# Kernel tuning notes

Hardware: AMD Instinct MI355X
Metric: run time of the kernel (lower is better)

The kernel has to match this reference:

```python
import jax, jax.numpy as jnp
import numpy as np

LN_EPS = 1e-12

def setup_inputs() -> dict:
    key = jax.random.key(0)
    k1, k2 = jax.random.split(key)
    B, S, H = 32, 2048, 1024
    input_tensor = jax.random.normal(k1, (B, S, H), dtype=jnp.float32)
    # learned params
    complex_weight = jax.random.normal(k2, (1, S // 2 + 1, H, 2), dtype=jnp.float32) * 0.02
    ln_gamma = jnp.ones((H,), dtype=jnp.float32)
    ln_beta = jnp.zeros((H,), dtype=jnp.float32)
    return {"input_tensor": input_tensor, "complex_weight": complex_weight,
            "ln_gamma": ln_gamma, "ln_beta": ln_beta}

def reference(input_tensor, complex_weight, ln_gamma, ln_beta):
    B, S, H = input_tensor.shape
    # FFT filter: rfft along seq, complex elementwise multiply, irfft
    x = jnp.fft.rfft(input_tensor, axis=1, norm='ortho')            # [B, S//2+1, H] complex64
    weight = complex_weight[..., 0] + 1j * complex_weight[..., 1]   # [1, S//2+1, H]
    x = x * weight
    seq_fft = jnp.fft.irfft(x, n=S, axis=1, norm='ortho')           # [B, S, H] real
    # dropout is identity in eval mode
    h = seq_fft + input_tensor
    # LayerNorm over last dim, eps=1e-12, biased variance (torch semantics)
    mean = jnp.mean(h, axis=-1, keepdims=True)
    var = jnp.mean(jnp.square(h - mean), axis=-1, keepdims=True)
    normed = (h - mean) * jax.lax.rsqrt(var + LN_EPS)
    return normed * ln_gamma + ln_beta
```

## Files before the change

kernel.cpp:

```cpp
#include <hip/hip_runtime.h>
#include <math.h>


#define PI_F 3.14159265358979323846f
#define SW(c) ((c) ^ (((c) >> 4) & 15))

__device__ __forceinline__ float2 cadd(float2 a, float2 b){ return make_float2(a.x+b.x, a.y+b.y); }
__device__ __forceinline__ float2 csub(float2 a, float2 b){ return make_float2(a.x-b.x, a.y-b.y); }
__device__ __forceinline__ float2 cmul(float2 a, float2 b){ return make_float2(a.x*b.x - a.y*b.y, a.x*b.y + a.y*b.x); }

template<int L>
__device__ __forceinline__ void fwd_stage(float2* A, int j){
  constexpr int half = L >> 1;
  const float ang0 = -PI_F / (float)L;
  #pragma unroll
  for (int r = 0; r < 4; ++r){
    int g    = j + (r << 7);
    int blk  = g / half;
    int joff = g - blk * half;
    int i0   = blk * (2 * L) + joff;
    float2 u0 = A[SW(i0)];
    float2 u1 = A[SW(i0 + half)];
    float2 u2 = A[SW(i0 + L)];
    float2 u3 = A[SW(i0 + L + half)];
    float sn, cs; __sincosf(ang0 * (float)joff, &sn, &cs);
    float2 w1 = make_float2(cs, sn);
    float2 t0  = cadd(u0, u2);
    float2 d02 = csub(u0, u2);
    float2 t1  = cadd(u1, u3);
    float2 d13 = csub(u1, u3);
    float2 t2  = cmul(d02, w1);
    float2 tm  = cmul(d13, w1);
    float2 t3  = make_float2(tm.y, -tm.x);
    float2 w2  = cmul(w1, w1);
    A[SW(i0)]            = cadd(t0, t1);
    A[SW(i0 + half)]     = cmul(csub(t0, t1), w2);
    A[SW(i0 + L)]        = cadd(t2, t3);
    A[SW(i0 + L + half)] = cmul(csub(t2, t3), w2);
  }
}

template<int l>
__device__ __forceinline__ void inv_stage(float2* A, int j){
  const float angB = PI_F / (float)(2 * l);
  #pragma unroll
  for (int r = 0; r < 4; ++r){
    int g    = j + (r << 7);
    int blk  = g / l;
    int joff = g - blk * l;
    int base = blk * (4 * l);
    int i0 = base + joff;
    float2 u0 = A[SW(i0)];
    float2 u1 = A[SW(i0 + l)];
    float2 u2 = A[SW(i0 + 2*l)];
    float2 u3 = A[SW(i0 + 3*l)];
    float sn, cs; __sincosf(angB * (float)joff, &sn, &cs);
    float2 wB = make_float2(cs, sn);
    float2 w  = cmul(wB, wB);
    float2 a1 = cmul(u1, w);
    float2 b0 = cadd(u0, a1), b1 = csub(u0, a1);
    float2 a3 = cmul(u3, w);
    float2 b2 = cadd(u2, a3), b3 = csub(u2, a3);
    float2 t2 = cmul(b2, wB);
    float2 c0 = cadd(b0, t2), c2 = csub(b0, t2);
    float2 iwB = make_float2(-wB.y, wB.x);
    float2 t3 = cmul(b3, iwB);
    float2 c1 = cadd(b1, t3), c3 = csub(b1, t3);
    A[SW(i0)]       = c0;
    A[SW(i0 + l)]   = c1;
    A[SW(i0 + 2*l)] = c2;
    A[SW(i0 + 3*l)] = c3;
  }
}

__device__ __forceinline__ float2 fetchW(const float2* __restrict__ wT,
                                         const float2* __restrict__ cw,
                                         int useT, int h, int k){
  if (useT) return wT[(size_t)h * 1025 + k];
  float2 w = cw[(size_t)k * 1024 + h];
  const float inv = 1.0f / 2048.0f;
  return make_float2((w.x + 1.0f) * inv, w.y * inv);
}

__global__ void prep_w_kernel(const float2* __restrict__ cw, float2* __restrict__ wT){
  __shared__ float2 tile[32][33];
  int k0 = blockIdx.x * 32, h0 = blockIdx.y * 32;
  int tx = threadIdx.x, ty = threadIdx.y;
  #pragma unroll
  for (int r = 0; r < 4; ++r){
    int k = k0 + ty + 8 * r;
    if (k < 1025) tile[ty + 8*r][tx] = cw[(size_t)k * 1024 + (h0 + tx)];
  }
  __syncthreads();
  const float inv = 1.0f / 2048.0f;
  #pragma unroll
  for (int r = 0; r < 4; ++r){
    int h = h0 + ty + 8 * r;
    int k = k0 + tx;
    if (k < 1025){
      float2 w = tile[tx][ty + 8*r];
      wT[(size_t)h * 1025 + k] = make_float2((w.x + 1.0f) * inv, w.y * inv);
    }
  }
}

__global__ __launch_bounds__(512) void fft_filter_kernel(
    const float2* __restrict__ x,
    const float2* __restrict__ cw,
    const float2* __restrict__ wT,
    int useT,
    float2* __restrict__ out){
  __shared__ float2 lds[4][2048];
  const int t  = threadIdx.x;
  const int bx = blockIdx.x;
  const int b  = bx >> 7;
  const int pg = bx & 127;
  const int f  = t >> 7;
  const int j  = t & 127;
  float2* A = lds[f];

  {
    const int p4 = t & 3, srow = t >> 2;
    const size_t base = ((size_t)b * 2048) * 512 + (size_t)(pg * 4 + p4);
    #pragma unroll
    for (int it = 0; it < 16; ++it){
      int s = srow + (it << 7);
      lds[p4][SW(s)] = x[base + (size_t)s * 512];
    }
  }
  __syncthreads();

  fwd_stage<1024>(A, j); __syncthreads();
  fwd_stage<256>(A, j);  __syncthreads();
  fwd_stage<64>(A, j);   __syncthreads();
  fwd_stage<16>(A, j);   __syncthreads();
  fwd_stage<4>(A, j);    __syncthreads();
  #pragma unroll
  for (int r = 0; r < 8; ++r){
    int m = j + (r << 7);
    int ia = SW(2*m), ib = SW(2*m + 1);
    float2 u = A[ia], v = A[ib];
    A[ia] = cadd(u, v);
    A[ib] = csub(u, v);
  }
  __syncthreads();

  {
    const int hA = (pg << 3) + (f << 1);
    if (j == 0){
      float2 z0 = A[0];
      float2 wa = fetchW(wT, cw, useT, hA, 0);
      float2 wb = fetchW(wT, cw, useT, hA + 1, 0);
      A[0] = make_float2(z0.x * wa.x, z0.y * wb.x);
      int p1 = SW(1);
      float2 zn = A[p1];
      wa = fetchW(wT, cw, useT, hA, 1024);
      wb = fetchW(wT, cw, useT, hA + 1, 1024);
      A[p1] = make_float2(zn.x * wa.x, zn.y * wb.x);
    }
    #pragma unroll
    for (int r = 0; r < 8; ++r){
      int k = 1 + j + (r << 7);
      if (k < 1024){
        int kr = 2048 - k;
        int p1 = SW((int)(__brev((unsigned)k) >> 21));
        int p2 = SW((int)(__brev((unsigned)kr) >> 21));
        float2 Z1 = A[p1], Z2 = A[p2];
        float2 Xa = make_float2(0.5f*(Z1.x + Z2.x), 0.5f*(Z1.y - Z2.y));
        float2 Xb = make_float2(0.5f*(Z1.y + Z2.y), 0.5f*(Z2.x - Z1.x));
        float2 wa = fetchW(wT, cw, useT, hA, k);
        float2 wb = fetchW(wT, cw, useT, hA + 1, k);
        float2 Ya = cmul(Xa, wa);
        float2 Yb = cmul(Xb, wb);
        A[p1] = make_float2(Ya.x - Yb.y, Ya.y + Yb.x);
        A[p2] = make_float2(Ya.x + Yb.y, Yb.x - Ya.y);
      }
    }
  }
  __syncthreads();

  #pragma unroll
  for (int r = 0; r < 8; ++r){
    int m = j + (r << 7);
    int ia = SW(2*m), ib = SW(2*m + 1);
    float2 u = A[ia], v = A[ib];
    A[ia] = cadd(u, v);
    A[ib] = csub(u, v);
  }
  __syncthreads();
  inv_stage<2>(A, j);   __syncthreads();
  inv_stage<8>(A, j);   __syncthreads();
  inv_stage<32>(A, j);  __syncthreads();
  inv_stage<128>(A, j); __syncthreads();
  inv_stage<512>(A, j); __syncthreads();

  {
    const int p4 = t & 3, srow = t >> 2;
    const size_t base = ((size_t)b * 2048) * 512 + (size_t)(pg * 4 + p4);
    #pragma unroll
    for (int it = 0; it < 16; ++it){
      int s = srow + (it << 7);
      out[base + (size_t)s * 512] = lds[p4][SW(s)];
    }
  }
}

__global__ __launch_bounds__(256) void ln_kernel(float* __restrict__ io,
                                                 const float* __restrict__ gma,
                                                 const float* __restrict__ bta){
  const int row = blockIdx.x;
  const int t = threadIdx.x;
  float4* r4 = (float4*)io + (size_t)row * 256;
  float4 v = r4[t];
  float s1 = v.x + v.y + v.z + v.w;
  float s2 = v.x*v.x + v.y*v.y + v.z*v.z + v.w*v.w;
  #pragma unroll
  for (int off = 32; off > 0; off >>= 1){
    s1 += __shfl_down(s1, off);
    s2 += __shfl_down(s2, off);
  }
  __shared__ float red[8];
  __shared__ float mr[2];
  const int wid = t >> 6, lane = t & 63;
  if (lane == 0){ red[wid] = s1; red[4 + wid] = s2; }
  __syncthreads();
  if (t == 0){
    float ts1 = red[0] + red[1] + red[2] + red[3];
    float ts2 = red[4] + red[5] + red[6] + red[7];
    float mean = ts1 * (1.0f / 1024.0f);
    float var  = ts2 * (1.0f / 1024.0f) - mean * mean;
    mr[0] = mean;
    mr[1] = rsqrtf(fmaxf(var, 0.0f) + 1e-12f);
  }
  __syncthreads();
  const float mean = mr[0], rstd = mr[1];
  const float4 gv = ((const float4*)gma)[t];
  const float4 bv = ((const float4*)bta)[t];
  float4 o;
  o.x = (v.x - mean) * rstd * gv.x + bv.x;
  o.y = (v.y - mean) * rstd * gv.y + bv.y;
  o.z = (v.z - mean) * rstd * gv.z + bv.z;
  o.w = (v.w - mean) * rstd * gv.w + bv.w;
  r4[t] = o;
}

extern "C" void kernel_launch(void* const* d_in, const int* in_sizes, int n_in,
                              void* d_out, int out_size, void* d_ws, size_t ws_size,
                              hipStream_t stream){
  const float2* x2  = (const float2*)d_in[0];
  const float2* cw2 = (const float2*)d_in[1];
  const float*  gma = (const float*)d_in[2];
  const float*  bta = (const float*)d_in[3];
  float2* out2 = (float2*)d_out;
  float*  outf = (float*)d_out;

  const int Bn = in_sizes[0] / (2048 * 1024);

  const size_t needW = (size_t)1025 * 1024 * sizeof(float2);
  const int useT = (ws_size >= needW) ? 1 : 0;
  float2* wT = (float2*)d_ws;

  if (useT){
    hipLaunchKernelGGL(prep_w_kernel, dim3(33, 32), dim3(32, 8), 0, stream, cw2, wT);
  }
  hipLaunchKernelGGL(fft_filter_kernel, dim3(Bn * 128), dim3(512), 0, stream,
                     x2, cw2, wT, useT, out2);
  hipLaunchKernelGGL(ln_kernel, dim3(Bn * 2048), dim3(256), 0, stream,
                     outf, gma, bta);
}
```

Before: 894.2 us.

## Halve FFT block width with float4 loads, XCD-aware mapping, wave-per-row layernorm

The FFT kernel now processes 4 hidden columns (two complex pairs) per 256-thread block instead of 8 columns per 512 threads. It loads and stores with float4 and remaps block indices so neighbouring column groups land on the same XCD for L2 locality. Launch bounds request 5 blocks per CU to raise occupancy. The layernorm kernel assigns one wavefront per row and reduces with xor shuffles, removing shared memory and block barriers, at the cost of narrower per-block memory segments in the FFT (16-byte columns strided by 4 KB).

```diff
diff --git a/kernel.cpp b/kernel.cpp
--- a/kernel.cpp
+++ b/kernel.cpp
@@ -104,28 +104,30 @@
   }
 }
 
-__global__ __launch_bounds__(512) void fft_filter_kernel(
-    const float2* __restrict__ x,
+__global__ __launch_bounds__(256, 5) void fft_filter_kernel(
+    const float4* __restrict__ x4,
     const float2* __restrict__ cw,
     const float2* __restrict__ wT,
     int useT,
-    float2* __restrict__ out){
-  __shared__ float2 lds[4][2048];
+    float4* __restrict__ out4){
+  __shared__ float2 lds[2][2048];
   const int t  = threadIdx.x;
-  const int bx = blockIdx.x;
-  const int b  = bx >> 7;
-  const int pg = bx & 127;
-  const int f  = t >> 7;
-  const int j  = t & 127;
+  const int bx  = blockIdx.x;
+  const int xcd = bx & 7;
+  const int ii  = bx >> 3;
+  const int b   = ii >> 5;
+  const int pg  = (xcd << 5) | (ii & 31);
+  const int f   = t >> 7;
+  const int j   = t & 127;
   float2* A = lds[f];
 
   {
-    const int p4 = t & 3, srow = t >> 2;
-    const size_t base = ((size_t)b * 2048) * 512 + (size_t)(pg * 4 + p4);
     #pragma unroll
-    for (int it = 0; it < 16; ++it){
-      int s = srow + (it << 7);
-      lds[p4][SW(s)] = x[base + (size_t)s * 512];
+    for (int it = 0; it < 8; ++it){
+      int s = t + (it << 8);
+      float4 v = x4[((size_t)b * 2048 + (size_t)s) * 256 + pg];
+      lds[0][SW(s)] = make_float2(v.x, v.y);
+      lds[1][SW(s)] = make_float2(v.z, v.w);
     }
   }
   __syncthreads();
@@ -146,7 +148,7 @@
   __syncthreads();
 
   {
-    const int hA = (pg << 3) + (f << 1);
+    const int hA = (pg << 2) + (f << 1);
     if (j == 0){
       float2 z0 = A[0];
       float2 wa = fetchW(wT, cw, useT, hA, 0);
@@ -195,12 +197,11 @@
   inv_stage<512>(A, j); __syncthreads();
 
   {
-    const int p4 = t & 3, srow = t >> 2;
-    const size_t base = ((size_t)b * 2048) * 512 + (size_t)(pg * 4 + p4);
     #pragma unroll
-    for (int it = 0; it < 16; ++it){
-      int s = srow + (it << 7);
-      out[base + (size_t)s * 512] = lds[p4][SW(s)];
+    for (int it = 0; it < 8; ++it){
+      int s = t + (it << 8);
+      float2 a = lds[0][SW(s)], c = lds[1][SW(s)];
+      out4[((size_t)b * 2048 + (size_t)s) * 256 + pg] = make_float4(a.x, a.y, c.x, c.y);
     }
   }
 }
@@ -208,50 +209,50 @@
 __global__ __launch_bounds__(256) void ln_kernel(float* __restrict__ io,
                                                  const float* __restrict__ gma,
                                                  const float* __restrict__ bta){
-  const int row = blockIdx.x;
-  const int t = threadIdx.x;
-  float4* r4 = (float4*)io + (size_t)row * 256;
-  float4 v = r4[t];
-  float s1 = v.x + v.y + v.z + v.w;
-  float s2 = v.x*v.x + v.y*v.y + v.z*v.z + v.w*v.w;
+  const int wid  = threadIdx.x >> 6;
+  const int lane = threadIdx.x & 63;
+  const size_t row = (size_t)blockIdx.x * 4 + (size_t)wid;
+  float4* r4 = (float4*)io + row * 256;
+  float4 v[4];
+  #pragma unroll
+  for (int q = 0; q < 4; ++q) v[q] = r4[lane + (q << 6)];
+  float s1 = 0.0f, s2 = 0.0f;
+  #pragma unroll
+  for (int q = 0; q < 4; ++q){
+    s1 += v[q].x + v[q].y + v[q].z + v[q].w;
+    s2 += v[q].x*v[q].x + v[q].y*v[q].y + v[q].z*v[q].z + v[q].w*v[q].w;
+  }
   #pragma unroll
   for (int off = 32; off > 0; off >>= 1){
-    s1 += __shfl_down(s1, off);
-    s2 += __shfl_down(s2, off);
-  }
-  __shared__ float red[8];
-  __shared__ float mr[2];
-  const int wid = t >> 6, lane = t & 63;
-  if (lane == 0){ red[wid] = s1; red[4 + wid] = s2; }
-  __syncthreads();
-  if (t == 0){
-    float ts1 = red[0] + red[1] + red[2] + red[3];
-    float ts2 = red[4] + red[5] + red[6] + red[7];
-    float mean = ts1 * (1.0f / 1024.0f);
-    float var  = ts2 * (1.0f / 1024.0f) - mean * mean;
-    mr[0] = mean;
-    mr[1] = rsqrtf(fmaxf(var, 0.0f) + 1e-12f);
-  }
-  __syncthreads();
-  const float mean = mr[0], rstd = mr[1];
-  const float4 gv = ((const float4*)gma)[t];
-  const float4 bv = ((const float4*)bta)[t];
-  float4 o;
-  o.x = (v.x - mean) * rstd * gv.x + bv.x;
-  o.y = (v.y - mean) * rstd * gv.y + bv.y;
-  o.z = (v.z - mean) * rstd * gv.z + bv.z;
-  o.w = (v.w - mean) * rstd * gv.w + bv.w;
-  r4[t] = o;
+    s1 += __shfl_xor(s1, off);
+    s2 += __shfl_xor(s2, off);
+  }
+  const float mean = s1 * (1.0f / 1024.0f);
+  const float var  = s2 * (1.0f / 1024.0f) - mean * mean;
+  const float rstd = rsqrtf(fmaxf(var, 0.0f) + 1e-12f);
+  const float4* g4 = (const float4*)gma;
+  const float4* b4 = (const float4*)bta;
+  #pragma unroll
+  for (int q = 0; q < 4; ++q){
+    float4 gv = g4[lane + (q << 6)];
+    float4 bv = b4[lane + (q << 6)];
+    float4 o;
+    o.x = (v[q].x - mean) * rstd * gv.x + bv.x;
+    o.y = (v[q].y - mean) * rstd * gv.y + bv.y;
+    o.z = (v[q].z - mean) * rstd * gv.z + bv.z;
+    o.w = (v[q].w - mean) * rstd * gv.w + bv.w;
+    r4[lane + (q << 6)] = o;
+  }
 }
 
 extern "C" void kernel_launch(void* const* d_in, const int* in_sizes, int n_in,
                               void* d_out, int out_size, void* d_ws, size_t ws_size,
                               hipStream_t stream){
-  const float2* x2  = (const float2*)d_in[0];
+  const float4* x4  = (const float4*)d_in[0];
   const float2* cw2 = (const float2*)d_in[1];
   const float*  gma = (const float*)d_in[2];
   const float*  bta = (const float*)d_in[3];
-  float2* out2 = (float2*)d_out;
+  float4* out4 = (float4*)d_out;
   float*  outf = (float*)d_out;
 
   const int Bn = in_sizes[0] / (2048 * 1024);
@@ -263,8 +264,8 @@
   if (useT){
     hipLaunchKernelGGL(prep_w_kernel, dim3(33, 32), dim3(32, 8), 0, stream, cw2, wT);
   }
-  hipLaunchKernelGGL(fft_filter_kernel, dim3(Bn * 128), dim3(512), 0, stream,
-                     x2, cw2, wT, useT, out2);
-  hipLaunchKernelGGL(ln_kernel, dim3(Bn * 2048), dim3(256), 0, stream,
+  hipLaunchKernelGGL(fft_filter_kernel, dim3(Bn * 256), dim3(256), 0, stream,
+                     x4, cw2, wT, useT, out4);
+  hipLaunchKernelGGL(ln_kernel, dim3(Bn * 512), dim3(256), 0, stream,
                      outf, gma, bta);
 }
```

Result: faster. 870.3 us (-2.7%).
